# Kernel optimization log

Measured on AMD Instinct MI355X. Metric: run time of the kernel, lower is better.

Reference implementation:

```python
import jax, jax.numpy as jnp
import numpy as np

OUT = 7          # output_size
SR = 2           # sampling_ratio
SCALE = 1.0 / 16.0  # 1 / feature_stride


def _context_boxes(boxes):
    """8 surrounding cells of a 3x3 grid around each RoI; offset-major concat ([8N,4])."""
    x1, y1, x2, y2 = boxes[:, 0], boxes[:, 1], boxes[:, 2], boxes[:, 3]
    w = (x2 - x1) / 3.0
    h = (y2 - y1) / 3.0
    offs = []
    for i in range(3):
        for j in range(3):
            if i == 1 and j == 1:
                continue
            dx = j * w
            dy = i * h
            offs.append(jnp.stack([x1 + dx, y1 + dy, x1 + dx + w, y1 + dy + h], axis=1))
    return jnp.concatenate(offs, axis=0)


def _roi_align_v2(feat, boxes, scale, out, sr):
    """ROIAlignV2 (aligned=True). feat [C,H,W], boxes [B,4] xyxy -> [B,C,out,out]."""
    C, H, W = feat.shape
    # aligned: half-pixel offset, no max(roi_size, 1)
    x1 = boxes[:, 0] * scale - 0.5
    y1 = boxes[:, 1] * scale - 0.5
    bw = (boxes[:, 2] * scale - 0.5 - x1) / out   # bin width
    bh = (boxes[:, 3] * scale - 0.5 - y1) / out   # bin height
    # sample positions along each axis: start + (bin + (s+0.5)/sr) * bin_size  -> [B, out*sr]
    g = jnp.arange(out * sr) // sr
    s = jnp.arange(out * sr) % sr
    t = g + (s + 0.5) / sr                         # [out*sr]
    ys = y1[:, None] + t[None, :] * bh[:, None]    # [B,S]
    xs = x1[:, None] + t[None, :] * bw[:, None]    # [B,S]

    def axis(p, size):
        valid = (p >= -1.0) & (p <= size)
        p = jnp.clip(p, 0.0, size - 1.0)
        lo = jnp.clip(jnp.floor(p), 0.0, size - 2.0).astype(jnp.int32)
        return lo, p - lo, valid

    yl, fy, vy = axis(ys, H)
    xl, fx, vx = axis(xs, W)
    Y = yl[:, :, None]          # [B,S,1]
    X = xl[:, None, :]          # [B,1,S]
    f00 = feat[:, Y, X]         # [C,B,S,S]
    f01 = feat[:, Y, X + 1]
    f10 = feat[:, Y + 1, X]
    f11 = feat[:, Y + 1, X + 1]
    wy = fy[:, :, None]
    wx = fx[:, None, :]
    v = (f00 * (1 - wy) * (1 - wx) + f01 * (1 - wy) * wx
         + f10 * wy * (1 - wx) + f11 * wy * wx)
    v = v * (vy[:, :, None] & vx[:, None, :]).astype(v.dtype)
    # average the sr x sr samples inside each output bin
    B = boxes.shape[0]
    v = v.reshape(C, B, out, sr, out, sr).mean(axis=(3, 5))
    return v.transpose(1, 0, 2, 3)  # [B,C,out,out]


def setup_inputs() -> dict:
    key = jax.random.key(0)
    k1, k2, k3, k4 = jax.random.split(key, 4)
    features = jax.random.normal(k1, (256, 64, 64), dtype=jnp.float32)  # stride-16 map of a 1024px image
    N = 128
    xy = jax.random.uniform(k2, (N, 2), minval=0.0, maxval=800.0)
    wh = jax.random.uniform(k3, (N, 2), minval=32.0, maxval=220.0)
    boxes = jnp.concatenate([xy, xy + wh], axis=1)                      # [N,4] xyxy, image coords
    w_fuse = jax.random.normal(k4, (256, 2048), dtype=jnp.float32) * 0.02  # Conv2d(2048,256,1) weight
    b_fuse = jnp.zeros((256,), dtype=jnp.float32)
    return {"features": features, "boxes": boxes, "w_fuse": w_fuse, "b_fuse": b_fuse}


def reference(features, boxes, w_fuse, b_fuse):
    N = boxes.shape[0]
    cboxes = _context_boxes(boxes)                               # [8N,4] offset-major
    pooled = _roi_align_v2(features, cboxes, SCALE, OUT, SR)     # [8N,256,7,7]
    chunk = pooled.reshape(N, -1, OUT, OUT)                      # faithful to torch .view(N,-1,7,7)
    out = jnp.einsum('nchw,oc->nohw', chunk, w_fuse) + b_fuse[None, :, None, None]
    return jax.nn.relu(out)                                      # [N,256,7,7]
```

## Files before the change

kernel.cpp:

```cpp
#include <hip/hip_runtime.h>
#include <hip/hip_fp16.h>

#define SCALE (1.0f/16.0f)

typedef __attribute__((ext_vector_type(8))) _Float16 f16x8;
typedef __attribute__((ext_vector_type(4))) float f32x4;
typedef __attribute__((ext_vector_type(16))) float f32x16;
typedef __attribute__((ext_vector_type(4))) unsigned int u32x4;
typedef unsigned int u32;

#define PIN16(W) { _Pragma("unroll") \
    for (int s_ = 0; s_ < 16; ++s_) \
        asm volatile("" : "+v"((W)[s_][0]), "+v"((W)[s_][1]), "+v"((W)[s_][2]), "+v"((W)[s_][3])); }

__device__ __forceinline__ void gload16(const void* g, void* l) {
    __builtin_amdgcn_global_load_lds(
        (const __attribute__((address_space(1))) unsigned int*)g,
        (__attribute__((address_space(3))) unsigned int*)l, 16, 0, 0);
}
__device__ __forceinline__ __half2 asH2(u32 v) {
    union { u32 i; __half2 h; } u; u.i = v; return u.h;
}
__device__ __forceinline__ u32 asU32(__half2 h) {
    union { __half2 h; u32 i; } u; u.h = h; return u.i;
}
__device__ __forceinline__ int dupH2(float f) {
    __half h = __float2half_rn(f);
    __half2 d; d.x = h; d.y = h;
    union { __half2 h2; int i; } u; u.h2 = d; return u.i;
}

__global__ void k_prep(const float* __restrict__ feat, __half* __restrict__ featT,
                       const float* __restrict__ wf, __half* __restrict__ wr) {
    __shared__ float t[64][65];
    int b = blockIdx.x;
    if (b < 256) {
        int cb = (b >> 6) << 6;
        int pb = (b & 63) << 6;
        int lx = threadIdx.x & 63, ly = threadIdx.x >> 6;
#pragma unroll
        for (int i = 0; i < 16; ++i) {
            int cl = i*4 + ly;
            t[cl][lx] = feat[(size_t)(cb + cl) * 4096 + pb + lx];
        }
        __syncthreads();
#pragma unroll
        for (int i = 0; i < 16; ++i) {
            int pl = i*4 + ly;
            featT[(size_t)(pb + pl) * 256 + cb + lx] = __float2half_rn(t[lx][pl]);
        }
    } else {
        int ch = (b - 256) * 256 + threadIdx.x;
        int l  = ch & 63;
        int sk = (ch >> 6) & 15;
        int ot = (ch >> 10) & 7;
        int j  = ch >> 13;
        int o = ot*32 + (l & 31);
        int k = j*256 + sk*16 + (l >> 5)*8;
        const float* src = wf + (size_t)o*2048 + k;
        f32x4 a = *(const f32x4*)src;
        f32x4 bb = *(const f32x4*)(src + 4);
        f16x8 p;
#pragma unroll
        for (int u = 0; u < 4; ++u) p[u] = (_Float16)a[u];
#pragma unroll
        for (int u = 0; u < 4; ++u) p[4+u] = (_Float16)bb[u];
        *((f16x8*)wr + ch) = p;
    }
}

__global__ void __launch_bounds__(256, 2) k_fused(
    const __half* __restrict__ featT,
    const float* __restrict__ boxes,
    const __half* __restrict__ wr,
    const float* __restrict__ bfuse,
    float* __restrict__ out)
{
    __shared__ char patch[28672];
    __shared__ char Pl[2][16384];
    __shared__ int4 tabs[4][2][7];
    __shared__ int  pbs[4][2];

    int tid = threadIdx.x;
    int lane = tid & 63, wid = tid >> 6;
    int r31 = lane & 31, l5 = lane >> 5;
    int oq = wid & 1, kh = wid >> 1;
    int bid = blockIdx.x;
    int n  = bid & 127;
    int hh = (bid >> 7) & 1;
    int oh = bid >> 8;
    int hw0 = hh * 25;
    int HWn = hh ? 24 : 25;

    int nb_base = (n & 15) * 8;
    int off = n >> 4;
    int t3 = off + (off >= 4 ? 1 : 0);
    int ci = t3 / 3, cj = t3 - ci*3;

    f32x16 acc0, acc1;
#pragma unroll
    for (int i = 0; i < 16; ++i) { acc0[i] = 0.f; acc1[i] = 0.f; }

    {
        int padrows = 32 - HWn;
        for (int i = tid; i < padrows*32*2; i += 256) {
            int b = i / (padrows*32);
            int rem = i - b*(padrows*32);
            int row = HWn + (rem >> 5), slot = rem & 31;
            *(u32x4*)(Pl[b] + row*512 + slot*16) = (u32x4){0,0,0,0};
        }
    }

    auto tablesW = [&](int jj, int isy, bool active) {
        if (active) {
            int nbx = nb_base + jj;
            float bx1 = boxes[nbx*4+0], by1 = boxes[nbx*4+1];
            float bx2 = boxes[nbx*4+2], by2 = boxes[nbx*4+3];
            float w3 = (bx2-bx1)*(1.f/3.f), h3 = (by2-by1)*(1.f/3.f);
            float org  = isy ? (by1 + ci*h3)*SCALE - 0.5f : (bx1 + cj*w3)*SCALE - 0.5f;
            float step = (isy ? h3 : w3) * (SCALE*(1.f/14.f));
            float sc = isy ? 0.25f : 1.f;
            float p = org + ((float)lane + 0.5f)*step;
            float pc = fminf(fmaxf(p, 0.f), 63.f);
            float fl = fminf(floorf(pc), 62.f);
            float fr = pc - fl;
            float c0 = __shfl(fl, 2*lane);
            float c1 = __shfl(fl, 2*lane+1);
            float f  = __shfl(fr, 2*lane);
            float f2 = __shfl(fr, 2*lane+1);
            float fl0 = __shfl(fl, 0);
            int base = min((int)fl0, 56);
            float d = c1 - c0;
            float a0 = sc*((1.f-f) + (1.f-d)*(1.f-f2));
            float a1 = sc*(f + (1.f-d)*f2 + d*(1.f-f2));
            float a2 = sc*(d*f2);
            if (lane < 7) {
                int4 e;
                e.x = (int)c0 - base;
                e.y = dupH2(a0); e.z = dupH2(a1); e.w = dupH2(a2);
                tabs[jj & 3][isy][lane] = e;
            }
            if (lane == 0) pbs[jj & 3][isy] = base;
        }
    };

    auto stage = [&](int jj) {
        int xb = pbs[jj & 3][0], yb = pbs[jj & 3][1];
#pragma unroll
        for (int i = 0; i < 7; ++i) {
            int seg = wid + 4*i;
            int row = seg >> 2, q = seg & 3;
            const __half* src = featT + ((size_t)((yb + row)*64 + xb))*256 + q*512 + lane*8;
            gload16(src, patch + row*4096 + q*1024);
        }
    };

    auto pool = [&](int jj) {
        int buf = jj & 1;
        int co = tid & 31;
        int e0 = tid >> 5;
        const char* pb = patch + co*16;
        for (int e = e0; e < HWn; e += 8) {
            int g = hw0 + e;
            int h = (g*37) >> 8, w = g - h*7;
            int4 tx = tabs[jj & 3][0][w], ty = tabs[jj & 3][1][h];
            int px0 = tx.x, py0 = ty.x;
            int lx2 = min(px0 + 2, 7), ly2 = min(py0 + 2, 6);
            const char* r0 = pb + (py0*8 + px0)*512;
            const char* r1 = pb + (min(py0+1,6)*8 + px0)*512;
            const char* r2 = pb + (ly2*8 + px0)*512;
            int dx2 = (lx2 - px0)*512;
            u32x4 F00 = *(const u32x4*)(r0);
            u32x4 F01 = *(const u32x4*)(r0 + 512);
            u32x4 F02 = *(const u32x4*)(r0 + dx2);
            u32x4 F10 = *(const u32x4*)(r1);
            u32x4 F11 = *(const u32x4*)(r1 + 512);
            u32x4 F12 = *(const u32x4*)(r1 + dx2);
            u32x4 F20 = *(const u32x4*)(r2);
            u32x4 F21 = *(const u32x4*)(r2 + 512);
            u32x4 F22 = *(const u32x4*)(r2 + dx2);
            __half2 xa = asH2(tx.y), xb2 = asH2(tx.z), xc = asH2(tx.w);
            __half2 ya = asH2(ty.y), yb2 = asH2(ty.z), yc = asH2(ty.w);
            u32x4 res;
#pragma unroll
            for (int s = 0; s < 4; ++s) {
                __half2 q0 = __hfma2(asH2(F02[s]), xc, __hfma2(asH2(F01[s]), xb2, __hmul2(asH2(F00[s]), xa)));
                __half2 q1 = __hfma2(asH2(F12[s]), xc, __hfma2(asH2(F11[s]), xb2, __hmul2(asH2(F10[s]), xa)));
                __half2 q2 = __hfma2(asH2(F22[s]), xc, __hfma2(asH2(F21[s]), xb2, __hmul2(asH2(F20[s]), xa)));
                res[s] = asU32(__hfma2(q2, yc, __hfma2(q1, yb2, __hmul2(q0, ya))));
            }
            *(u32x4*)(Pl[buf] + e*512 + ((co*16) ^ ((e & 31) << 4))) = res;
        }
    };

    u32x4 WfA[16], WfB[16];
    auto prefW = [&](u32x4* dst, int j) {
#pragma unroll
        for (int t = 0; t < 2; ++t) {
            int otg = oh*4 + oq*2 + t;
            const u32x4* wb = (const u32x4*)wr + ((size_t)((j*8 + otg)*16 + kh*8))*64 + lane;
#pragma unroll
            for (int s = 0; s < 8; ++s) dst[t*8 + s] = wb[s*64];
        }
    };

    auto gemm = [&](const u32x4* Wsrc, int j) {
        const char* plb = (j & 1) ? Pl[1] : Pl[0];
        f16x8 pf[8];
#pragma unroll
        for (int s = 0; s < 8; ++s) {
            int sk = kh*8 + s;
            int byo = r31*512 + ((sk*32 + l5*16) ^ (r31 << 4));
            pf[s] = *(const f16x8*)(plb + byo);
        }
#pragma unroll
        for (int s = 0; s < 8; ++s) {
            acc0 = __builtin_amdgcn_mfma_f32_32x32x16_f16(
                __builtin_bit_cast(f16x8, Wsrc[s]), pf[s], acc0, 0, 0, 0);
            acc1 = __builtin_amdgcn_mfma_f32_32x32x16_f16(
                __builtin_bit_cast(f16x8, Wsrc[8 + s]), pf[s], acc1, 0, 0, 0);
        }
    };

    tablesW(wid >> 1, wid & 1, wid < 4);
    __syncthreads();
    stage(0);
    prefW(WfA, 0);
    PIN16(WfA);
    __syncthreads();
    pool(0);
    __syncthreads();

#pragma unroll
    for (int j = 0; j < 8; ++j) {
        gemm((j & 1) ? WfB : WfA, j);
        if (j < 7) {
            stage(j+1);
            prefW((j & 1) ? WfA : WfB, j+1);
            if (j & 1) { PIN16(WfA); } else { PIN16(WfB); }
        }
        __syncthreads();
        if (j < 7) pool(j+1);
        if (j < 6) tablesW(j+2, wid, wid < 2);
        __syncthreads();
    }

    float* red = (float*)patch;
    if (kh == 1) {
#pragma unroll
        for (int t = 0; t < 2; ++t) {
            f32x16 a = t ? acc1 : acc0;
#pragma unroll
            for (int q4 = 0; q4 < 4; ++q4) {
                f32x4 v;
#pragma unroll
                for (int i = 0; i < 4; ++i) v[i] = a[q4*4 + i];
                *(f32x4*)((char*)red + (oq*2 + t)*4096 + r31*128 + q4*32 + l5*16) = v;
            }
        }
    }
    __syncthreads();
    if (kh == 0) {
        int hw = hw0 + r31;
        bool ok = r31 < HWn;
        float* ob = out + (size_t)n*12544 + hw;
#pragma unroll
        for (int t = 0; t < 2; ++t) {
            f32x16 a = t ? acc1 : acc0;
            int otb = oh*128 + (oq*2 + t)*32;
#pragma unroll
            for (int q4 = 0; q4 < 4; ++q4) {
                f32x4 r = *(const f32x4*)((const char*)red + (oq*2 + t)*4096 + r31*128 + q4*32 + l5*16);
#pragma unroll
                for (int i = 0; i < 4; ++i) {
                    int o = otb + q4*8 + l5*4 + i;
                    float v = a[q4*4 + i] + r[i] + bfuse[o];
                    if (ok) ob[(size_t)o*49] = fmaxf(v, 0.f);
                }
            }
        }
    }
}

extern "C" void kernel_launch(void* const* d_in, const int* in_sizes, int n_in,
                              void* d_out, int out_size, void* d_ws, size_t ws_size,
                              hipStream_t stream) {
    const float* feat  = (const float*)d_in[0];
    const float* boxes = (const float*)d_in[1];
    const float* wf    = (const float*)d_in[2];
    const float* bfuse = (const float*)d_in[3];
    float* out = (float*)d_out;

    char* ws = (char*)d_ws;
    __half* wr    = (__half*)ws;
    __half* featT = (__half*)(ws + (1u<<20));

    k_prep<<<512, 256, 0, stream>>>(feat, featT, wf, wr);
    k_fused<<<512, 256, 0, stream>>>(featT, boxes, wr, bfuse, out);
}
```

Measured before the change: 36.63 us.

## Split fused RoI-align GEMM block into producer and consumer warps

```diff
diff --git a/kernel.cpp b/kernel.cpp
--- a/kernel.cpp
+++ b/kernel.cpp
@@ -69,14 +69,14 @@
     }
 }
 
-__global__ void __launch_bounds__(256, 2) k_fused(
+__global__ void __launch_bounds__(512) k_fused(
     const __half* __restrict__ featT,
     const float* __restrict__ boxes,
     const __half* __restrict__ wr,
     const float* __restrict__ bfuse,
     float* __restrict__ out)
 {
-    __shared__ char patch[28672];
+    __shared__ char patch[2][28672];
     __shared__ char Pl[2][16384];
     __shared__ int4 tabs[4][2][7];
     __shared__ int  pbs[4][2];
@@ -84,26 +84,21 @@
     int tid = threadIdx.x;
     int lane = tid & 63, wid = tid >> 6;
     int r31 = lane & 31, l5 = lane >> 5;
-    int oq = wid & 1, kh = wid >> 1;
     int bid = blockIdx.x;
     int n  = bid & 127;
-    int hh = (bid >> 7) & 1;
-    int oh = bid >> 8;
-    int hw0 = hh * 25;
-    int HWn = hh ? 24 : 25;
+    int hh = bid >> 7;
+    int hw0 = hh * 32;
+    int HWn = hh ? 17 : 32;
+    bool producer = wid < 4;
 
     int nb_base = (n & 15) * 8;
     int off = n >> 4;
     int t3 = off + (off >= 4 ? 1 : 0);
     int ci = t3 / 3, cj = t3 - ci*3;
 
-    f32x16 acc0, acc1;
-#pragma unroll
-    for (int i = 0; i < 16; ++i) { acc0[i] = 0.f; acc1[i] = 0.f; }
-
     {
         int padrows = 32 - HWn;
-        for (int i = tid; i < padrows*32*2; i += 256) {
+        for (int i = tid; i < padrows*32*2; i += 512) {
             int b = i / (padrows*32);
             int rem = i - b*(padrows*32);
             int row = HWn + (rem >> 5), slot = rem & 31;
@@ -146,12 +141,13 @@
 
     auto stage = [&](int jj) {
         int xb = pbs[jj & 3][0], yb = pbs[jj & 3][1];
+        char* pd = patch[jj & 1];
 #pragma unroll
         for (int i = 0; i < 7; ++i) {
             int seg = wid + 4*i;
             int row = seg >> 2, q = seg & 3;
             const __half* src = featT + ((size_t)((yb + row)*64 + xb))*256 + q*512 + lane*8;
-            gload16(src, patch + row*4096 + q*1024);
+            gload16(src, pd + row*4096 + q*1024);
         }
     };
 
@@ -159,7 +155,7 @@
         int buf = jj & 1;
         int co = tid & 31;
         int e0 = tid >> 5;
-        const char* pb = patch + co*16;
+        const char* pb = patch[buf] + co*16;
         for (int e = e0; e < HWn; e += 8) {
             int g = hw0 + e;
             int h = (g*37) >> 8, w = g - h*7;
@@ -193,90 +189,72 @@
         }
     };
 
-    u32x4 WfA[16], WfB[16];
-    auto prefW = [&](u32x4* dst, int j) {
+    int cw = wid - 4;
+    u32x4 Wf[32];
+    f32x16 acc0, acc1;
+#pragma unroll
+    for (int i = 0; i < 16; ++i) { acc0[i] = 0.f; acc1[i] = 0.f; }
+
+    auto prefW_half = [&](int j, int sb) {
 #pragma unroll
         for (int t = 0; t < 2; ++t) {
-            int otg = oh*4 + oq*2 + t;
-            const u32x4* wb = (const u32x4*)wr + ((size_t)((j*8 + otg)*16 + kh*8))*64 + lane;
-#pragma unroll
-            for (int s = 0; s < 8; ++s) dst[t*8 + s] = wb[s*64];
-        }
-    };
-
-    auto gemm = [&](const u32x4* Wsrc, int j) {
+            int otg = cw*2 + t;
+            const u32x4* wb = (const u32x4*)wr + ((size_t)((j*8 + otg)*16))*64 + lane;
+#pragma unroll
+            for (int s = 0; s < 8; ++s) Wf[t*16 + sb*8 + s] = wb[(sb*8 + s)*64];
+        }
+    };
+
+    auto gemm_half = [&](int j, int sb) {
         const char* plb = (j & 1) ? Pl[1] : Pl[0];
-        f16x8 pf[8];
 #pragma unroll
         for (int s = 0; s < 8; ++s) {
-            int sk = kh*8 + s;
+            int sk = sb*8 + s;
             int byo = r31*512 + ((sk*32 + l5*16) ^ (r31 << 4));
-            pf[s] = *(const f16x8*)(plb + byo);
-        }
-#pragma unroll
-        for (int s = 0; s < 8; ++s) {
+            f16x8 pf = *(const f16x8*)(plb + byo);
             acc0 = __builtin_amdgcn_mfma_f32_32x32x16_f16(
-                __builtin_bit_cast(f16x8, Wsrc[s]), pf[s], acc0, 0, 0, 0);
+                __builtin_bit_cast(f16x8, Wf[sk]), pf, acc0, 0, 0, 0);
             acc1 = __builtin_amdgcn_mfma_f32_32x32x16_f16(
-                __builtin_bit_cast(f16x8, Wsrc[8 + s]), pf[s], acc1, 0, 0, 0);
-        }
-    };
-
-    tablesW(wid >> 1, wid & 1, wid < 4);
+                __builtin_bit_cast(f16x8, Wf[16 + sk]), pf, acc1, 0, 0, 0);
+        }
+    };
+
+    if (wid < 2) { tablesW(0, wid, true); tablesW(1, wid, true); tablesW(2, wid, true); }
     __syncthreads();
-    stage(0);
-    prefW(WfA, 0);
-    PIN16(WfA);
+    if (producer) { stage(0); stage(1); }
+    else          { prefW_half(0, 0); prefW_half(0, 1); PIN16(Wf); PIN16((Wf+16)); }
     __syncthreads();
-    pool(0);
+    if (producer) pool(0);
     __syncthreads();
 
 #pragma unroll
     for (int j = 0; j < 8; ++j) {
-        gemm((j & 1) ? WfB : WfA, j);
-        if (j < 7) {
-            stage(j+1);
-            prefW((j & 1) ? WfA : WfB, j+1);
-            if (j & 1) { PIN16(WfA); } else { PIN16(WfB); }
+        if (producer) {
+            if (j < 6) stage(j+2);
+            if (j < 7) pool(j+1);
+            if (j < 5) tablesW(j+3, wid, wid < 2);
+        } else {
+            gemm_half(j, 0);
+            if (j < 7) prefW_half(j+1, 0);
+            gemm_half(j, 1);
+            if (j < 7) { prefW_half(j+1, 1); PIN16(Wf); PIN16((Wf+16)); }
         }
         __syncthreads();
-        if (j < 7) pool(j+1);
-        if (j < 6) tablesW(j+2, wid, wid < 2);
-        __syncthreads();
-    }
-
-    float* red = (float*)patch;
-    if (kh == 1) {
-#pragma unroll
-        for (int t = 0; t < 2; ++t) {
-            f32x16 a = t ? acc1 : acc0;
-#pragma unroll
-            for (int q4 = 0; q4 < 4; ++q4) {
-                f32x4 v;
-#pragma unroll
-                for (int i = 0; i < 4; ++i) v[i] = a[q4*4 + i];
-                *(f32x4*)((char*)red + (oq*2 + t)*4096 + r31*128 + q4*32 + l5*16) = v;
-            }
-        }
-    }
-    __syncthreads();
-    if (kh == 0) {
+    }
+
+    if (!producer) {
         int hw = hw0 + r31;
         bool ok = r31 < HWn;
         float* ob = out + (size_t)n*12544 + hw;
 #pragma unroll
         for (int t = 0; t < 2; ++t) {
             f32x16 a = t ? acc1 : acc0;
-            int otb = oh*128 + (oq*2 + t)*32;
-#pragma unroll
-            for (int q4 = 0; q4 < 4; ++q4) {
-                f32x4 r = *(const f32x4*)((const char*)red + (oq*2 + t)*4096 + r31*128 + q4*32 + l5*16);
-#pragma unroll
-                for (int i = 0; i < 4; ++i) {
-                    int o = otb + q4*8 + l5*4 + i;
-                    float v = a[q4*4 + i] + r[i] + bfuse[o];
-                    if (ok) ob[(size_t)o*49] = fmaxf(v, 0.f);
-                }
+            int otb = (cw*2 + t)*32;
+#pragma unroll
+            for (int reg = 0; reg < 16; ++reg) {
+                int o = otb + (reg & 3) + 8*(reg >> 2) + 4*l5;
+                float v = a[reg] + bfuse[o];
+                if (ok) ob[(size_t)o*49] = fmaxf(v, 0.f);
             }
         }
     }
@@ -296,5 +274,5 @@
     __half* featT = (__half*)(ws + (1u<<20));
 
     k_prep<<<512, 256, 0, stream>>>(feat, featT, wf, wr);
-    k_fused<<<512, 256, 0, stream>>>(featT, boxes, wr, bfuse, out);
-}
+    k_fused<<<256, 512, 0, stream>>>(featT, boxes, wr, bfuse, out);
+}
```

Measured after the change: 30.37 us. 1.21x faster.
